# Performance work log

Measured on AMD Instinct MI355X. Metric: run time of the kernel, lower is better.

The kernel has to match this reference:

```python
import jax, jax.numpy as jnp
import numpy as np

N_NODES = 100000
N_EDGES = 1600000
N_GRAPHS = 1000
D_IN = 64
D_HID = 64
D_OUT = 8


def _glorot(k, shape):
    lim = float(np.sqrt(6.0 / (shape[0] + shape[1])))
    return jax.random.uniform(k, shape, jnp.float32, -lim, lim)


def setup_inputs() -> dict:
    key = jax.random.key(0)
    ks = jax.random.split(key, 12)
    x = jax.random.normal(ks[0], (N_NODES, D_IN), jnp.float32)
    edge_index = jax.random.randint(ks[1], (2, N_EDGES), 0, N_NODES, jnp.int32)
    batch = jnp.sort(jax.random.randint(ks[2], (N_NODES,), 0, N_GRAPHS, jnp.int32))
    return {
        "x": x,
        "edge_index": edge_index,
        "batch": batch,
        "W1": _glorot(ks[3], (D_IN, D_HID)),
        "b1": jnp.zeros((D_HID,), jnp.float32),
        "W2": _glorot(ks[4], (D_HID, D_HID)),
        "b2": jnp.zeros((D_HID,), jnp.float32),
        "lw1": _glorot(ks[5], (D_HID, D_HID // 2)),
        "lb1": jnp.zeros((D_HID // 2,), jnp.float32),
        "lw2": _glorot(ks[6], (D_HID // 2, D_OUT)),
        "lb2": jnp.zeros((D_OUT,), jnp.float32),
    }


def reference(x, edge_index, batch, W1, b1, W2, b2, lw1, lb1, lw2, lb2):
    # --- GCN normalization (PyG defaults: add self-loops, sym norm) ---
    loop = jnp.arange(N_NODES, dtype=edge_index.dtype)
    src = jnp.concatenate([edge_index[0], loop])
    dst = jnp.concatenate([edge_index[1], loop])
    deg = jax.ops.segment_sum(jnp.ones_like(dst, jnp.float32), dst, num_segments=N_NODES)
    dinv = jnp.where(deg > 0, jax.lax.rsqrt(jnp.maximum(deg, 1.0)), 0.0)
    norm = dinv[src] * dinv[dst]  # [E+N]

    def gcn_conv(h, W, b):
        h = h @ W  # [N, d]
        msg = h[src] * norm[:, None]  # gather along edges
        return jax.ops.segment_sum(msg, dst, num_segments=N_NODES) + b

    h = jax.nn.relu(gcn_conv(x, W1, b1))
    h = gcn_conv(h, W2, b2)

    # --- global mean pool per graph ---
    counts = jax.ops.segment_sum(jnp.ones((N_NODES,), jnp.float32), batch, num_segments=N_GRAPHS)
    pooled = jax.ops.segment_sum(h, batch, num_segments=N_GRAPHS) / jnp.maximum(counts, 1.0)[:, None]

    # --- MLP head (dropout = identity in eval) ---
    z = jax.nn.relu(pooled @ lw1 + lb1)
    return z @ lw2 + lb2
```

## Files before the change

kernel.cpp:

```cpp
#include <hip/hip_runtime.h>

static constexpr int NN  = 100000;
static constexpr int NE  = 1600000;
static constexpr int NG  = 1000;
static constexpr int D   = 64;
static constexpr int DH  = 32;
static constexpr int DO  = 8;
static constexpr int BKT = 128;
static constexpr int NBK = (NN + BKT - 1) / BKT;
static constexpr int CAP = 2560;
static constexpr int CHUNK = 4096;
static constexpr int NCH = (NE + CHUNK - 1) / CHUNK;
static constexpr int MAXW = 13504;
static constexpr int MAPS = MAXW * 8;
static constexpr int NBAND = ((NN - 1) >> 9) + 1;

typedef __attribute__((ext_vector_type(8))) short bf16x8;
typedef __attribute__((ext_vector_type(4))) float f32x4;

__device__ __forceinline__ float b2f(unsigned short u) {
    return __uint_as_float(((unsigned int)u) << 16);
}
__device__ __forceinline__ unsigned short f2b(float f) {
    unsigned int u = __float_as_uint(f);
    u += 0x7FFFu + ((u >> 16) & 1u);
    return (unsigned short)(u >> 16);
}
__device__ __forceinline__ uint4 pack8(const unsigned short* h) {
    uint4 u;
    u.x = (unsigned)h[0] | ((unsigned)h[1] << 16);
    u.y = (unsigned)h[2] | ((unsigned)h[3] << 16);
    u.z = (unsigned)h[4] | ((unsigned)h[5] << 16);
    u.w = (unsigned)h[6] | ((unsigned)h[7] << 16);
    return u;
}

__global__ __launch_bounds__(1024) void
k_prepw(const float* __restrict__ W1, const float* __restrict__ W2,
        const int* __restrict__ batch,
        unsigned short* __restrict__ wtbuf, int* __restrict__ gcur,
        int* __restrict__ lbg, int* __restrict__ wbase, int* __restrict__ map) {
    __shared__ int bnd[NG + 1];
    __shared__ int tsum[256];
    int t = threadIdx.x;
    int b = blockIdx.x;
    if (b == 0) {
        for (int i = t; i < NBK; i += 1024) gcur[i] = 0;
    } else if (b == 3) {
        for (int g = t; g <= NG; g += 1024) {
            int lo = 0, hi = NN;
            while (lo < hi) { int m = (lo + hi) >> 1; if (batch[m] < g) lo = m + 1; else hi = m; }
            bnd[g] = lo;
        }
        __syncthreads();
        int s = 0, loc[4];
        if (t < 256) {
#pragma unroll
            for (int j = 0; j < 4; ++j) {
                int g = t * 4 + j;
                int pw = (g < NG) ? ((bnd[g + 1] - bnd[g] + 7) >> 3) : 0;
                loc[j] = s; s += pw;
            }
            tsum[t] = s;
        }
        __syncthreads();
        for (int o = 1; o < 256; o <<= 1) {
            int a = (t < 256 && t >= o) ? tsum[t - o] : 0;
            __syncthreads();
            if (t < 256) tsum[t] += a;
            __syncthreads();
        }
        if (t < 256) {
            int base = (t > 0) ? tsum[t - 1] : 0;
#pragma unroll
            for (int j = 0; j < 4; ++j) {
                int g = t * 4 + j;
                if (g < NG) wbase[g] = base + loc[j];
            }
            if (t == 255) wbase[NG] = tsum[255];
        }
        if (t <= NG) lbg[t] = bnd[t];
    } else if (b >= 4) {
        int4 m4 = {-1, -1, -1, -1};
        for (int i = (b - 4) * 1024 + t; i < MAPS / 4; i += 8 * 1024)
            ((int4*)map)[i] = m4;
    } else {
        if (t < 256) {
            const float* W = (b == 2) ? W2 : W1;
            unsigned short* WtHi = wtbuf + (size_t)(b - 1) * 8192;
            unsigned short* WtLo = WtHi + 4096;
            int n = t >> 2, k0 = (t & 3) * 16;
            unsigned short hi[16], lo[16];
#pragma unroll
            for (int i = 0; i < 16; ++i) {
                float v = W[(k0 + i) * 64 + n];
                hi[i] = f2b(v);
                lo[i] = f2b(v - b2f(hi[i]));
            }
            ((uint4*)WtHi)[n * 8 + (t & 3) * 2]     = pack8(hi);
            ((uint4*)WtHi)[n * 8 + (t & 3) * 2 + 1] = pack8(hi + 8);
            ((uint4*)WtLo)[n * 8 + (t & 3) * 2]     = pack8(lo);
            ((uint4*)WtLo)[n * 8 + (t & 3) * 2 + 1] = pack8(lo + 8);
        }
    }
}

__global__ __launch_bounds__(128) void
k_fillmap(const int* __restrict__ lbg, const int* __restrict__ wbase,
          int* __restrict__ map) {
    int g = blockIdx.x;
    int base = wbase[g] * 8;
    int lb = lbg[g], n = lbg[g + 1] - lb;
    int padded = (n + 7) & ~7;
    for (int i = threadIdx.x; i < padded; i += 128)
        map[base + i] = (i < n) ? (lb + i) : -1;
}

__global__ __launch_bounds__(512) void
k_bin(const int* __restrict__ src, const int* __restrict__ dst,
      int* __restrict__ gcur, int* __restrict__ ebuf) {
    __shared__ int lcnt[NBK];
    __shared__ int lbase[NBK];
    int t = threadIdx.x;
    long base = (long)blockIdx.x * CHUNK;
    for (int b = t; b < NBK; b += 512) lcnt[b] = 0;
    __syncthreads();
    int pk[8], bk[8], of[8];
#pragma unroll
    for (int j = 0; j < 8; ++j) {
        long i = base + j * 512 + t;
        if (i < NE) {
            int d = dst[i];
            bk[j] = d >> 7;
            pk[j] = src[i] * BKT + (d & (BKT - 1));
            of[j] = atomicAdd(&lcnt[bk[j]], 1);
        } else bk[j] = -1;
    }
    __syncthreads();
    for (int b = t; b < NBK; b += 512) {
        int c = lcnt[b];
        if (c) lbase[b] = b * CAP + atomicAdd(&gcur[b], c);
    }
    __syncthreads();
#pragma unroll
    for (int j = 0; j < 8; ++j)
        if (bk[j] >= 0) ebuf[lbase[bk[j]] + of[j]] = pk[j];
}

__global__ __launch_bounds__(512) void
k_csrdeg(const int* __restrict__ gcur, const int* __restrict__ ebuf,
         int* __restrict__ rowptr, int* __restrict__ deg, float* __restrict__ dinv,
         int* __restrict__ csr) {
    __shared__ int earr[CAP];
    __shared__ int esrt[CAP];
    __shared__ int hist[BKT];
    __shared__ int sc[BKT];
    __shared__ int lcur[BKT];
    __shared__ int bh[NBAND];
    __shared__ int bs[NBAND];
    int b = blockIdx.x, t = threadIdx.x;
    if (t < BKT) hist[t] = 0;
    for (int i = t; i < NBAND; i += 512) bh[i] = 0;
    __syncthreads();
    int beg = b * CAP;
    int cnt = gcur[b];
    for (int e = t; e < cnt; e += 512) {
        int p = ebuf[beg + e];
        earr[e] = p;
        atomicAdd(&hist[p & (BKT - 1)], 1);
        atomicAdd(&bh[p >> 16], 1);
    }
    __syncthreads();
    if (t < BKT) sc[t] = hist[t];
    if (t < NBAND) bs[t] = bh[t];
    __syncthreads();
    for (int o = 1; o < 256; o <<= 1) {
        int a1 = (t < BKT && t >= o) ? sc[t - o] : 0;
        int a2 = (t < NBAND && t >= o) ? bs[t - o] : 0;
        __syncthreads();
        if (t < BKT) sc[t] += a1;
        if (t < NBAND) bs[t] += a2;
        __syncthreads();
    }
    if (t < NBAND) bh[t] = bs[t] - bh[t];
    int v0 = b * BKT;
    if (t < BKT) {
        int v = v0 + t;
        if (v < NN) {
            int excl = beg + sc[t] - hist[t];
            rowptr[v] = excl;
            deg[v]    = hist[t];
            dinv[v]   = rsqrtf((float)(hist[t] + 1));
            lcur[t]   = excl;
        }
    }
    __syncthreads();
    for (int e = t; e < cnt; e += 512) {
        int p = earr[e];
        int pos = atomicAdd(&bh[p >> 16], 1);
        esrt[pos] = p;
    }
    __syncthreads();
    for (int base2 = 0; base2 < cnt; base2 += 512) {
        int e = base2 + t;
        int p = (e < cnt) ? esrt[e] : -1;
        if (p >= 0) {
            int slot = atomicAdd(&lcur[p & (BKT - 1)], 1);
            csr[slot] = p >> 7;
        }
        __syncthreads();
    }
}

__global__ __launch_bounds__(256) void
k_mm_mfma(const float* __restrict__ Ain, const unsigned short* __restrict__ wt,
          const float* __restrict__ dinv, uint4* __restrict__ out) {
    __shared__ unsigned short smem[4 * 64 * 72];
    unsigned short* Ahi  = smem;
    unsigned short* Alo  = smem + 4608;
    unsigned short* WtHi = smem + 9216;
    unsigned short* WtLo = smem + 13824;
    int t = threadIdx.x;
    int r = t >> 2, cc = t & 3, c0 = cc * 16;
    long n0 = (long)blockIdx.x * 64;
    {
        const uint4* H = (const uint4*)wt;
        const uint4* L = (const uint4*)(wt + 4096);
        uint4* dh = (uint4*)&WtHi[r * 72 + c0];
        uint4* dl = (uint4*)&WtLo[r * 72 + c0];
        dh[0] = H[r * 8 + cc * 2]; dh[1] = H[r * 8 + cc * 2 + 1];
        dl[0] = L[r * 8 + cc * 2]; dl[1] = L[r * 8 + cc * 2 + 1];
    }
    {
        long n = n0 + r; if (n >= NN) n = NN - 1;
        const float4* X = (const float4*)Ain;
        unsigned short hi[16], lo[16];
#pragma unroll
        for (int i = 0; i < 4; ++i) {
            float4 v = X[n * 16 + cc * 4 + i];
            float vv[4] = {v.x, v.y, v.z, v.w};
#pragma unroll
            for (int j = 0; j < 4; ++j) {
                unsigned short h = f2b(vv[j]);
                hi[i * 4 + j] = h;
                lo[i * 4 + j] = f2b(vv[j] - b2f(h));
            }
        }
        uint4* dh = (uint4*)&Ahi[r * 72 + c0];
        uint4* dl = (uint4*)&Alo[r * 72 + c0];
        dh[0] = pack8(hi); dh[1] = pack8(hi + 8);
        dl[0] = pack8(lo); dl[1] = pack8(lo + 8);
    }
    __syncthreads();
    int lane = t & 63, w = t >> 6;
    int q = lane >> 4, m = lane & 15;
    f32x4 acc[4] = {{0.f,0.f,0.f,0.f},{0.f,0.f,0.f,0.f},{0.f,0.f,0.f,0.f},{0.f,0.f,0.f,0.f}};
#pragma unroll
    for (int s = 0; s < 2; ++s) {
        int ko = s * 32 + q * 8;
        bf16x8 ah = *(const bf16x8*)&Ahi[(w * 16 + m) * 72 + ko];
        bf16x8 al = *(const bf16x8*)&Alo[(w * 16 + m) * 72 + ko];
#pragma unroll
        for (int c = 0; c < 4; ++c) {
            bf16x8 bh = *(const bf16x8*)&WtHi[(c * 16 + m) * 72 + ko];
            bf16x8 bl = *(const bf16x8*)&WtLo[(c * 16 + m) * 72 + ko];
            acc[c] = __builtin_amdgcn_mfma_f32_16x16x32_bf16(ah, bh, acc[c], 0, 0, 0);
            acc[c] = __builtin_amdgcn_mfma_f32_16x16x32_bf16(ah, bl, acc[c], 0, 0, 0);
            acc[c] = __builtin_amdgcn_mfma_f32_16x16x32_bf16(al, bh, acc[c], 0, 0, 0);
        }
    }
    __syncthreads();
    float* Ct = (float*)smem;
#pragma unroll
    for (int c = 0; c < 4; ++c)
#pragma unroll
        for (int rr = 0; rr < 4; ++rr)
            Ct[(w * 16 + q * 4 + rr) * 68 + c * 16 + m] = acc[c][rr];
    __syncthreads();
    {
        long n = n0 + r;
        if (n < NN) {
            float dv = dinv[n];
            unsigned short ob[16];
#pragma unroll
            for (int i = 0; i < 4; ++i) {
                float4 v = *(const float4*)&Ct[r * 68 + c0 + i * 4];
                ob[i * 4 + 0] = f2b(v.x * dv); ob[i * 4 + 1] = f2b(v.y * dv);
                ob[i * 4 + 2] = f2b(v.z * dv); ob[i * 4 + 3] = f2b(v.w * dv);
            }
            out[n * 8 + cc * 2]     = pack8(ob);
            out[n * 8 + cc * 2 + 1] = pack8(ob + 8);
        }
    }
}

__global__ __launch_bounds__(512) void
k_aggmm(const int* __restrict__ rowptr, const int* __restrict__ deg,
        const int* __restrict__ csr,
        const uint4* __restrict__ g4, const float* __restrict__ dinv,
        const float* __restrict__ bias, const unsigned short* __restrict__ wt,
        uint4* __restrict__ out) {
    __shared__ unsigned short smem[3 * 4608];
    unsigned short* Ahi  = smem;
    unsigned short* WtHi = smem + 4608;
    unsigned short* WtLo = smem + 9216;
    int t = threadIdx.x;
    long n0 = (long)blockIdx.x * 64;
    if (t < 256) {
        int r = t >> 2, cc = t & 3, c0 = cc * 16;
        const uint4* H = (const uint4*)wt;
        const uint4* L = (const uint4*)(wt + 4096);
        uint4* dh = (uint4*)&WtHi[r * 72 + c0];
        uint4* dl = (uint4*)&WtLo[r * 72 + c0];
        dh[0] = H[r * 8 + cc * 2]; dh[1] = H[r * 8 + cc * 2 + 1];
        dl[0] = L[r * 8 + cc * 2]; dl[1] = L[r * 8 + cc * 2 + 1];
    }
    int lane = t & 63, w = t >> 6;
    int fg = lane & 7, slot = lane >> 3;
    int ln = w * 8 + slot;
    long v = n0 + ln;
    int vc = (v < NN) ? (int)v : NN - 1;
    int beg = rowptr[vc];
    int len = (v < NN) ? deg[vc] : 0;
    int lmax = len;
    lmax = max(lmax, __shfl_xor(lmax, 8));
    lmax = max(lmax, __shfl_xor(lmax, 16));
    lmax = max(lmax, __shfl_xor(lmax, 32));
    float acc[8];
    {
        uint4 sv = g4[(long)vc * 8 + fg];
        if (v >= NN) { sv.x = sv.y = sv.z = sv.w = 0u; }
        acc[0] = __uint_as_float(sv.x << 16); acc[1] = __uint_as_float(sv.x & 0xFFFF0000u);
        acc[2] = __uint_as_float(sv.y << 16); acc[3] = __uint_as_float(sv.y & 0xFFFF0000u);
        acc[4] = __uint_as_float(sv.z << 16); acc[5] = __uint_as_float(sv.z & 0xFFFF0000u);
        acc[6] = __uint_as_float(sv.w << 16); acc[7] = __uint_as_float(sv.w & 0xFFFF0000u);
    }
    for (int e = 0; e < lmax; e += 8) {
#pragma unroll
        for (int j = 0; j < 8; ++j) {
            int ee = e + j;
            float m = (ee < len) ? 1.f : 0.f;
            int idx = beg + ((ee < len) ? ee : 0);
            int srcn = csr[idx];
            uint4 a = g4[(long)srcn * 8 + fg];
            acc[0] += m * __uint_as_float(a.x << 16);
            acc[1] += m * __uint_as_float(a.x & 0xFFFF0000u);
            acc[2] += m * __uint_as_float(a.y << 16);
            acc[3] += m * __uint_as_float(a.y & 0xFFFF0000u);
            acc[4] += m * __uint_as_float(a.z << 16);
            acc[5] += m * __uint_as_float(a.z & 0xFFFF0000u);
            acc[6] += m * __uint_as_float(a.w << 16);
            acc[7] += m * __uint_as_float(a.w & 0xFFFF0000u);
        }
    }
    {
        float dv = dinv[vc];
        unsigned short ob[8];
#pragma unroll
        for (int k = 0; k < 8; ++k) {
            float x = fmaxf(acc[k] * dv + bias[fg * 8 + k], 0.f);
            ob[k] = f2b(x);
        }
        *(uint4*)&Ahi[ln * 72 + fg * 8] = pack8(ob);
    }
    __syncthreads();
    int q = lane >> 4, m = lane & 15;
    int rs = (w & 3) * 16;
    int cb0 = (w >> 2) * 2;
    f32x4 c2[2] = {{0.f,0.f,0.f,0.f},{0.f,0.f,0.f,0.f}};
#pragma unroll
    for (int s = 0; s < 2; ++s) {
        int ko = s * 32 + q * 8;
        bf16x8 ah = *(const bf16x8*)&Ahi[(rs + m) * 72 + ko];
#pragma unroll
        for (int c = 0; c < 2; ++c) {
            bf16x8 bh = *(const bf16x8*)&WtHi[((cb0 + c) * 16 + m) * 72 + ko];
            bf16x8 bl = *(const bf16x8*)&WtLo[((cb0 + c) * 16 + m) * 72 + ko];
            c2[c] = __builtin_amdgcn_mfma_f32_16x16x32_bf16(ah, bh, c2[c], 0, 0, 0);
            c2[c] = __builtin_amdgcn_mfma_f32_16x16x32_bf16(ah, bl, c2[c], 0, 0, 0);
        }
    }
    __syncthreads();
    float* Ct = (float*)smem;
#pragma unroll
    for (int c = 0; c < 2; ++c)
#pragma unroll
        for (int rr = 0; rr < 4; ++rr)
            Ct[(rs + q * 4 + rr) * 68 + (cb0 + c) * 16 + m] = c2[c][rr];
    __syncthreads();
    {
        int r = t >> 3, c8 = (t & 7) * 8;
        long n = n0 + r;
        if (n < NN) {
            float dv = dinv[n];
            float4 a = *(const float4*)&Ct[r * 68 + c8];
            float4 b = *(const float4*)&Ct[r * 68 + c8 + 4];
            unsigned short ob[8] = {f2b(a.x * dv), f2b(a.y * dv), f2b(a.z * dv), f2b(a.w * dv),
                                    f2b(b.x * dv), f2b(b.y * dv), f2b(b.z * dv), f2b(b.w * dv)};
            out[n * 8 + (t & 7)] = pack8(ob);
        }
    }
}

__global__ __launch_bounds__(256) void
k_agg2pool(const int* __restrict__ rowptr, const int* __restrict__ deg,
           const int* __restrict__ csr,
           const uint4* __restrict__ g4, const float* __restrict__ dinv,
           const int* __restrict__ map, float* __restrict__ partial) {
    int t = threadIdx.x;
    int lane = t & 63;
    int fg = lane & 7;
    int slot = lane >> 3;
    int w = blockIdx.x * 4 + (t >> 6);
    int v = map[w * 8 + slot];
    int vc = (v < 0) ? 0 : v;
    int beg = rowptr[vc];
    int len = (v < 0) ? 0 : deg[vc];
    int lmax = len;
    lmax = max(lmax, __shfl_xor(lmax, 8));
    lmax = max(lmax, __shfl_xor(lmax, 16));
    lmax = max(lmax, __shfl_xor(lmax, 32));
    float acc[8];
    {
        uint4 sv = g4[(long)vc * 8 + fg];
        if (v < 0) { sv.x = sv.y = sv.z = sv.w = 0u; }
        acc[0] = __uint_as_float(sv.x << 16); acc[1] = __uint_as_float(sv.x & 0xFFFF0000u);
        acc[2] = __uint_as_float(sv.y << 16); acc[3] = __uint_as_float(sv.y & 0xFFFF0000u);
        acc[4] = __uint_as_float(sv.z << 16); acc[5] = __uint_as_float(sv.z & 0xFFFF0000u);
        acc[6] = __uint_as_float(sv.w << 16); acc[7] = __uint_as_float(sv.w & 0xFFFF0000u);
    }
    for (int e = 0; e < lmax; e += 8) {
#pragma unroll
        for (int j = 0; j < 8; ++j) {
            int ee = e + j;
            float m = (ee < len) ? 1.f : 0.f;
            int idx2 = beg + ((ee < len) ? ee : 0);
            int srcn = csr[idx2];
            uint4 a = g4[(long)srcn * 8 + fg];
            acc[0] += m * __uint_as_float(a.x << 16);
            acc[1] += m * __uint_as_float(a.x & 0xFFFF0000u);
            acc[2] += m * __uint_as_float(a.y << 16);
            acc[3] += m * __uint_as_float(a.y & 0xFFFF0000u);
            acc[4] += m * __uint_as_float(a.z << 16);
            acc[5] += m * __uint_as_float(a.z & 0xFFFF0000u);
            acc[6] += m * __uint_as_float(a.w << 16);
            acc[7] += m * __uint_as_float(a.w & 0xFFFF0000u);
        }
    }
    float dv = dinv[vc];
#pragma unroll
    for (int k = 0; k < 8; ++k) {
        acc[k] *= dv;
        acc[k] += __shfl_xor(acc[k], 8);
        acc[k] += __shfl_xor(acc[k], 16);
        acc[k] += __shfl_xor(acc[k], 32);
    }
    if (slot == 0) {
        float4* p4 = (float4*)&partial[(long)w * 64];
        f32x4 a = {acc[0], acc[1], acc[2], acc[3]};
        f32x4 b = {acc[4], acc[5], acc[6], acc[7]};
        p4[fg * 2]     = *(float4*)&a;
        p4[fg * 2 + 1] = *(float4*)&b;
    }
}

__global__ void k_head(const float* __restrict__ partial,
                       const int* __restrict__ lbg, const int* __restrict__ wbase,
                       const float* __restrict__ b2,
                       const float* __restrict__ lw1, const float* __restrict__ lb1,
                       const float* __restrict__ lw2, const float* __restrict__ lb2,
                       float* __restrict__ out) {
    __shared__ float pl[D];
    __shared__ float z[DH];
    int g = blockIdx.x;
    int t = threadIdx.x;
    int w0 = wbase[g], w1 = wbase[g + 1];
    int cnt = lbg[g + 1] - lbg[g];
    float s = 0.f;
    for (int w = w0; w < w1; ++w) s += partial[(long)w * 64 + t];
    pl[t] = (cnt > 0) ? (s / (float)cnt + b2[t]) : 0.f;
    __syncthreads();
    if (t < DH) {
        float a = lb1[t];
#pragma unroll
        for (int k = 0; k < D; ++k) a += pl[k] * lw1[k * DH + t];
        z[t] = fmaxf(a, 0.f);
    }
    __syncthreads();
    if (t < DO) {
        float a = lb2[t];
#pragma unroll
        for (int j = 0; j < DH; ++j) a += z[j] * lw2[j * DO + t];
        out[g * DO + t] = a;
    }
}

extern "C" void kernel_launch(void* const* d_in, const int* in_sizes, int n_in,
                              void* d_out, int out_size, void* d_ws, size_t ws_size,
                              hipStream_t stream) {
    const float* x    = (const float*)d_in[0];
    const int*   ei   = (const int*)  d_in[1];
    const int*   batch= (const int*)  d_in[2];
    const float* W1   = (const float*)d_in[3];
    const float* b1   = (const float*)d_in[4];
    const float* W2   = (const float*)d_in[5];
    const float* b2   = (const float*)d_in[6];
    const float* lw1  = (const float*)d_in[7];
    const float* lb1  = (const float*)d_in[8];
    const float* lw2  = (const float*)d_in[9];
    const float* lb2  = (const float*)d_in[10];
    float* out = (float*)d_out;

    const int* srcv = ei;
    const int* dstv = ei + NE;

    char* ws = (char*)d_ws;
    size_t off = 0;
    auto alloc = [&](size_t bytes) {
        void* p = ws + off;
        off = (off + bytes + 255) & ~(size_t)255;
        return p;
    };
    int*   gcur   = (int*)  alloc((size_t)NBK * 4);
    int*   rowptr = (int*)  alloc((size_t)NN * 4);
    int*   deg    = (int*)  alloc((size_t)NN * 4);
    int*   csr    = (int*)  alloc((size_t)NBK * CAP * 4);
    float* dinv   = (float*)alloc((size_t)NN * 4);
    int*   lbg    = (int*)  alloc((size_t)(NG + 1) * 4);
    int*   wbase  = (int*)  alloc((size_t)(NG + 1) * 4);
    int*   map    = (int*)  alloc((size_t)MAPS * 4);
    float* partial= (float*)alloc((size_t)MAXW * D * 4);
    unsigned short* wtbuf = (unsigned short*)alloc((size_t)4 * 4096 * 2);
    unsigned short* bufA = (unsigned short*)alloc((size_t)NN * D * 2);
    unsigned short* bufB = (unsigned short*)alloc((size_t)NN * D * 2);
    int*   ebuf   = (int*)bufA;

    k_prepw  <<<12, 1024, 0, stream>>>(W1, W2, batch, wtbuf, gcur, lbg, wbase, map);
    k_fillmap<<<NG, 128, 0, stream>>>(lbg, wbase, map);
    k_bin    <<<NCH, 512, 0, stream>>>(srcv, dstv, gcur, ebuf);
    k_csrdeg <<<NBK, 512, 0, stream>>>(gcur, ebuf, rowptr, deg, dinv, csr);

    const int MMB = (NN + 63) / 64;

    k_mm_mfma<<<MMB, 256, 0, stream>>>(x, wtbuf, dinv, (uint4*)bufA);
    k_aggmm<<<MMB, 512, 0, stream>>>(rowptr, deg, csr, (const uint4*)bufA, dinv, b1,
                                     wtbuf + 8192, (uint4*)bufB);
    k_agg2pool<<<MAXW / 4, 256, 0, stream>>>(rowptr, deg, csr, (const uint4*)bufB, dinv,
                                             map, partial);
    k_head<<<NG, 64, 0, stream>>>(partial, lbg, wbase, b2, lw1, lb1, lw2, lb2, out);
}
```

Baseline: 212.1 us.

## Split layer-2 features into four planes and aggregate each plane separately

The layer-2 matmul output is now written as four 16-feature bf16 planes of 32 bytes per node rather than one interleaved 128-byte row. The aggregation-pool kernel runs four phases, one per plane, with each lane handling 4 features. Each phase's gather therefore touches a 3.2MB plane that fits better in cache, which targets L2/MALL misses on random neighbour gathers. The CSR index loads become nontemporal. The trade-off is that edge indices and rowptr are re-read four times, and the gathers become narrower 8-byte requests.

New measurement: 272.5 us. +28.5%, slower.

```diff
diff --git a/kernel.cpp b/kernel.cpp
--- a/kernel.cpp
+++ b/kernel.cpp
@@ -14,6 +14,7 @@
 static constexpr int MAXW = 13504;
 static constexpr int MAPS = MAXW * 8;
 static constexpr int NBAND = ((NN - 1) >> 9) + 1;
+static constexpr int PBLK = MAXW / 8;
 
 typedef __attribute__((ext_vector_type(8))) short bf16x8;
 typedef __attribute__((ext_vector_type(4))) float f32x4;
@@ -341,7 +342,7 @@
             int ee = e + j;
             float m = (ee < len) ? 1.f : 0.f;
             int idx = beg + ((ee < len) ? ee : 0);
-            int srcn = csr[idx];
+            int srcn = __builtin_nontemporal_load(&csr[idx]);
             uint4 a = g4[(long)srcn * 8 + fg];
             acc[0] += m * __uint_as_float(a.x << 16);
             acc[1] += m * __uint_as_float(a.x & 0xFFFF0000u);
@@ -389,78 +390,72 @@
             Ct[(rs + q * 4 + rr) * 68 + (cb0 + c) * 16 + m] = c2[c][rr];
     __syncthreads();
     {
-        int r = t >> 3, c8 = (t & 7) * 8;
+        int r = t >> 3, c = t & 7;
         long n = n0 + r;
         if (n < NN) {
             float dv = dinv[n];
-            float4 a = *(const float4*)&Ct[r * 68 + c8];
-            float4 b = *(const float4*)&Ct[r * 68 + c8 + 4];
+            float4 a = *(const float4*)&Ct[r * 68 + c * 8];
+            float4 b = *(const float4*)&Ct[r * 68 + c * 8 + 4];
             unsigned short ob[8] = {f2b(a.x * dv), f2b(a.y * dv), f2b(a.z * dv), f2b(a.w * dv),
                                     f2b(b.x * dv), f2b(b.y * dv), f2b(b.z * dv), f2b(b.w * dv)};
-            out[n * 8 + (t & 7)] = pack8(ob);
+            int p = c >> 1, qq = c & 1;
+            out[(size_t)p * (NN * 2) + n * 2 + qq] = pack8(ob);
         }
     }
 }
 
 __global__ __launch_bounds__(256) void
-k_agg2pool(const int* __restrict__ rowptr, const int* __restrict__ deg,
-           const int* __restrict__ csr,
-           const uint4* __restrict__ g4, const float* __restrict__ dinv,
-           const int* __restrict__ map, float* __restrict__ partial) {
+k_agg2p(const int* __restrict__ rowptr, const int* __restrict__ deg,
+        const int* __restrict__ csr, const uint2* __restrict__ g2p,
+        const float* __restrict__ dinv, const int* __restrict__ map,
+        float* __restrict__ partial) {
     int t = threadIdx.x;
+    int bid = blockIdx.x;
+    int phase = bid / PBLK;
+    int blk   = bid - phase * PBLK;
+    const uint2* plane = g2p + (size_t)phase * NN * 4;
     int lane = t & 63;
-    int fg = lane & 7;
-    int slot = lane >> 3;
-    int w = blockIdx.x * 4 + (t >> 6);
-    int v = map[w * 8 + slot];
+    int part = lane & 3;
+    int slot = (lane >> 2) & 7;
+    int grp  = blk * 8 + (t >> 5);
+    int v = map[grp * 8 + slot];
     int vc = (v < 0) ? 0 : v;
     int beg = rowptr[vc];
     int len = (v < 0) ? 0 : deg[vc];
     int lmax = len;
+    lmax = max(lmax, __shfl_xor(lmax, 4));
     lmax = max(lmax, __shfl_xor(lmax, 8));
     lmax = max(lmax, __shfl_xor(lmax, 16));
-    lmax = max(lmax, __shfl_xor(lmax, 32));
-    float acc[8];
-    {
-        uint4 sv = g4[(long)vc * 8 + fg];
-        if (v < 0) { sv.x = sv.y = sv.z = sv.w = 0u; }
-        acc[0] = __uint_as_float(sv.x << 16); acc[1] = __uint_as_float(sv.x & 0xFFFF0000u);
-        acc[2] = __uint_as_float(sv.y << 16); acc[3] = __uint_as_float(sv.y & 0xFFFF0000u);
-        acc[4] = __uint_as_float(sv.z << 16); acc[5] = __uint_as_float(sv.z & 0xFFFF0000u);
-        acc[6] = __uint_as_float(sv.w << 16); acc[7] = __uint_as_float(sv.w & 0xFFFF0000u);
+    float a0, a1, a2, a3;
+    {
+        uint2 sv = plane[(size_t)vc * 4 + part];
+        if (v < 0) { sv.x = sv.y = 0u; }
+        a0 = __uint_as_float(sv.x << 16); a1 = __uint_as_float(sv.x & 0xFFFF0000u);
+        a2 = __uint_as_float(sv.y << 16); a3 = __uint_as_float(sv.y & 0xFFFF0000u);
     }
     for (int e = 0; e < lmax; e += 8) {
 #pragma unroll
         for (int j = 0; j < 8; ++j) {
             int ee = e + j;
             float m = (ee < len) ? 1.f : 0.f;
-            int idx2 = beg + ((ee < len) ? ee : 0);
-            int srcn = csr[idx2];
-            uint4 a = g4[(long)srcn * 8 + fg];
-            acc[0] += m * __uint_as_float(a.x << 16);
-            acc[1] += m * __uint_as_float(a.x & 0xFFFF0000u);
-            acc[2] += m * __uint_as_float(a.y << 16);
-            acc[3] += m * __uint_as_float(a.y & 0xFFFF0000u);
-            acc[4] += m * __uint_as_float(a.z << 16);
-            acc[5] += m * __uint_as_float(a.z & 0xFFFF0000u);
-            acc[6] += m * __uint_as_float(a.w << 16);
-            acc[7] += m * __uint_as_float(a.w & 0xFFFF0000u);
+            int idx = beg + ((ee < len) ? ee : 0);
+            int srcn = __builtin_nontemporal_load(&csr[idx]);
+            uint2 a = plane[(size_t)srcn * 4 + part];
+            a0 += m * __uint_as_float(a.x << 16);
+            a1 += m * __uint_as_float(a.x & 0xFFFF0000u);
+            a2 += m * __uint_as_float(a.y << 16);
+            a3 += m * __uint_as_float(a.y & 0xFFFF0000u);
         }
     }
     float dv = dinv[vc];
-#pragma unroll
-    for (int k = 0; k < 8; ++k) {
-        acc[k] *= dv;
-        acc[k] += __shfl_xor(acc[k], 8);
-        acc[k] += __shfl_xor(acc[k], 16);
-        acc[k] += __shfl_xor(acc[k], 32);
-    }
+    a0 *= dv; a1 *= dv; a2 *= dv; a3 *= dv;
+    a0 += __shfl_xor(a0, 4);  a0 += __shfl_xor(a0, 8);  a0 += __shfl_xor(a0, 16);
+    a1 += __shfl_xor(a1, 4);  a1 += __shfl_xor(a1, 8);  a1 += __shfl_xor(a1, 16);
+    a2 += __shfl_xor(a2, 4);  a2 += __shfl_xor(a2, 8);  a2 += __shfl_xor(a2, 16);
+    a3 += __shfl_xor(a3, 4);  a3 += __shfl_xor(a3, 8);  a3 += __shfl_xor(a3, 16);
     if (slot == 0) {
-        float4* p4 = (float4*)&partial[(long)w * 64];
-        f32x4 a = {acc[0], acc[1], acc[2], acc[3]};
-        f32x4 b = {acc[4], acc[5], acc[6], acc[7]};
-        p4[fg * 2]     = *(float4*)&a;
-        p4[fg * 2 + 1] = *(float4*)&b;
+        float4 w4 = {a0, a1, a2, a3};
+        *(float4*)&partial[(size_t)grp * 64 + phase * 16 + part * 4] = w4;
     }
 }
 
@@ -545,7 +540,7 @@
     k_mm_mfma<<<MMB, 256, 0, stream>>>(x, wtbuf, dinv, (uint4*)bufA);
     k_aggmm<<<MMB, 512, 0, stream>>>(rowptr, deg, csr, (const uint4*)bufA, dinv, b1,
                                      wtbuf + 8192, (uint4*)bufB);
-    k_agg2pool<<<MAXW / 4, 256, 0, stream>>>(rowptr, deg, csr, (const uint4*)bufB, dinv,
-                                             map, partial);
+    k_agg2p<<<4 * PBLK, 256, 0, stream>>>(rowptr, deg, csr, (const uint2*)bufB, dinv,
+                                          map, partial);
     k_head<<<NG, 64, 0, stream>>>(partial, lbg, wbase, b2, lw1, lb1, lw2, lb2, out);
 }
```
